# Kernel tuning notes

Hardware: AMD Instinct MI355X
Metric: run time of the kernel (lower is better)

## Reference

```python
import jax, jax.numpy as jnp
import numpy as np
from jax import lax

WHISPER_DIM, WAVLM_DIM, MUQ_DIM = 1280, 1024, 1024
CODEBOOK_SIZE, CODEBOOK_DIM = 8192, 256
B, T_W, T_M = 8, 2048, 1024  # T_w = T_wl = 2048 @50Hz, muq @25Hz -> T_m = 1024
CONCAT_DIM = WHISPER_DIM + WAVLM_DIM + MUQ_DIM


def setup_inputs() -> dict:
    key = jax.random.key(0)
    ks = jax.random.split(key, 10)
    s = 0.02
    return {
        "whisper_feat": jax.random.normal(ks[0], (B, T_W, WHISPER_DIM), jnp.float32),
        "wavlm_feat": jax.random.normal(ks[1], (B, T_W, WAVLM_DIM), jnp.float32),
        "muq_feat": jax.random.normal(ks[2], (B, T_M, MUQ_DIM), jnp.float32),
        # Conv1d weights, torch layout (out_ch, in_ch, k)
        "w_conv_w": jax.random.normal(ks[3], (WHISPER_DIM, WHISPER_DIM, 4), jnp.float32) * s,
        "w_conv_b": jnp.zeros((WHISPER_DIM,), jnp.float32),
        "wl_conv_w": jax.random.normal(ks[4], (WAVLM_DIM, WAVLM_DIM, 4), jnp.float32) * s,
        "wl_conv_b": jnp.zeros((WAVLM_DIM,), jnp.float32),
        # Linear: torch layout (out_features, in_features)
        "proj_w": jax.random.normal(ks[5], (CODEBOOK_DIM, CONCAT_DIM), jnp.float32) * s,
        "proj_b": jnp.zeros((CODEBOOK_DIM,), jnp.float32),
        "codebook": jax.random.normal(ks[6], (CODEBOOK_SIZE, CODEBOOK_DIM), jnp.float32) * 0.02,
    }


def _conv1d_s2(x_btc, w_oik, b):
    # x: (B, T, C) -> (B, C, T) conv k=4 s=2 p=1 -> (B, T//2, C)
    y = lax.conv_general_dilated(
        x_btc.transpose(0, 2, 1), w_oik,
        window_strides=(2,), padding=[(1, 1)],
        dimension_numbers=("NCH", "OIH", "NCH"))
    return (y + b[None, :, None]).transpose(0, 2, 1)


def reference(whisper_feat, wavlm_feat, muq_feat, w_conv_w, w_conv_b,
              wl_conv_w, wl_conv_b, proj_w, proj_b, codebook):
    w = _conv1d_s2(whisper_feat, w_conv_w, w_conv_b)   # (B, 1024, 1280)
    wl = _conv1d_s2(wavlm_feat, wl_conv_w, wl_conv_b)  # (B, 1024, 1024)
    m = muq_feat                                        # (B, 1024, 1024)
    min_len = min(w.shape[1], wl.shape[1], m.shape[1])
    concat = jnp.concatenate([w[:, :min_len], wl[:, :min_len], m[:, :min_len]], axis=-1)
    z_e = jnp.einsum("btc,dc->btd", concat, proj_w) + proj_b  # (B, T, D)

    # VQ: squared-Euclidean argmin against the codebook (same argmin as cdist)
    Bsz, T, D = z_e.shape
    z_flat = z_e.reshape(-1, D)
    d2 = (jnp.sum(z_flat * z_flat, axis=-1, keepdims=True)
          - 2.0 * z_flat @ codebook.T
          + jnp.sum(codebook * codebook, axis=-1)[None, :])  # (B*T, K)
    codes = jnp.argmin(d2, axis=-1)                     # (B*T,)
    z_q = codebook[codes].reshape(Bsz, T, D)
    z_q_st = z_e + lax.stop_gradient(z_q - z_e)
    commit_loss = jnp.mean(jnp.square(z_e - lax.stop_gradient(z_q)))
    return z_q_st, codes.reshape(Bsz, T), commit_loss
```

## Files before the change

### kernel.cpp

```cpp
#include <hip/hip_runtime.h>
#include <cstdint>
#include <cstddef>

typedef unsigned short u16;
typedef __attribute__((ext_vector_type(8))) short bf16x8;
typedef __attribute__((ext_vector_type(4))) float f32x4;
typedef unsigned int u32;
typedef __attribute__((address_space(1))) const u32 gu32;
typedef __attribute__((address_space(3))) u32 lu32;

__device__ __forceinline__ void gload_lds16(const void* g, void* l) {
    __builtin_amdgcn_global_load_lds((gu32*)g, (lu32*)l, 16, 0, 0);
}

__device__ __forceinline__ u16 f2bf(float v) {
    u32 u = __float_as_uint(v);
    return (u16)((u + 0x7fffu + ((u >> 16) & 1u)) >> 16);
}
__device__ __forceinline__ float bf2f(u16 h) { return __uint_as_float(((u32)h) << 16); }

__device__ __forceinline__ void split3(float f, u16& h1, u16& h2, u16& h3) {
    h1 = f2bf(f); float r = f - bf2f(h1);
    h2 = f2bf(r); r -= bf2f(h2);
    h3 = f2bf(r);
}

__device__ __forceinline__ void mfma6(f32x4& c, bf16x8 a1, bf16x8 a2, bf16x8 a3,
                                      bf16x8 b1, bf16x8 b2, bf16x8 b3) {
    c = __builtin_amdgcn_mfma_f32_16x16x32_bf16(a1, b1, c, 0, 0, 0);
    c = __builtin_amdgcn_mfma_f32_16x16x32_bf16(a1, b2, c, 0, 0, 0);
    c = __builtin_amdgcn_mfma_f32_16x16x32_bf16(a2, b1, c, 0, 0, 0);
    c = __builtin_amdgcn_mfma_f32_16x16x32_bf16(a1, b3, c, 0, 0, 0);
    c = __builtin_amdgcn_mfma_f32_16x16x32_bf16(a3, b1, c, 0, 0, 0);
    c = __builtin_amdgcn_mfma_f32_16x16x32_bf16(a2, b2, c, 0, 0, 0);
}

__global__ __launch_bounds__(256)
void split_x8t(const float* __restrict__ x, u16* __restrict__ p0,
               size_t pstr, int I) {
    __shared__ u16 tl[12288];
    const int b = blockIdx.x / 33, blk = blockIdx.x - b * 33;
    const int o0 = blk * 64;
    const int nval = (o0 + 64 <= 2050) ? 64 : (2050 - o0);
    const int c0 = blockIdx.y << 6;
    const int tid = threadIdx.x;
    const int r = tid >> 2, c4 = tid & 3;

    if (r < nval) {
        int local = o0 + r;
        int parity = local >= 1025 ? 1 : 0;
        int idx = local - parity * 1025;
        int prow = 2 * idx + parity;
        bool pad = (prow == 0) || (prow == 2049);
        int s = pad ? 0 : (prow - 1);
        const float* src = x + (size_t)(b * 2048 + s) * I + c0;
#pragma unroll
        for (int k = 0; k < 4; k++) {
            int cf4 = c4 + k * 4;
            float4 v = make_float4(0.f, 0.f, 0.f, 0.f);
            if (!pad) v = *reinterpret_cast<const float4*>(src + cf4 * 4);
            float vals[4] = {v.x, v.y, v.z, v.w};
            int base = ((cf4 >> 1) * 64 + r) * 8 + (cf4 & 1) * 4;
#pragma unroll
            for (int q = 0; q < 4; q++) {
                u16 h1, h2, h3; split3(vals[q], h1, h2, h3);
                tl[base + q]        = h1;
                tl[4096 + base + q] = h2;
                tl[8192 + base + q] = h3;
            }
        }
    }
    __syncthreads();
#pragma unroll
    for (int e = tid; e < 1536; e += 256) {
        int p = e >> 9, rem = e & 511;
        int gs = rem >> 6, rr = rem & 63;
        if (rr < nval) {
            size_t dst = (size_t)p * pstr +
                         (size_t)((c0 >> 3) + gs) * 131200 +
                         (size_t)(b * 2050 + o0 + rr) * 8;
            *reinterpret_cast<bf16x8*>(&p0[dst]) =
                *reinterpret_cast<const bf16x8*>(&tl[p * 4096 + (gs * 64 + rr) * 8]);
        }
    }
}

__global__ __launch_bounds__(256)
void split_rows8t(const float* __restrict__ in, u16* __restrict__ p0,
                  size_t pstr, int R, int C) {
    __shared__ u16 tl[12288];
    const int r0 = blockIdx.x << 6;
    const int c0 = blockIdx.y << 6;
    const int tid = threadIdx.x;
    const int r = tid >> 2, c4 = tid & 3;
    const float* src = in + (size_t)(r0 + r) * C + c0;
#pragma unroll
    for (int k = 0; k < 4; k++) {
        int cf4 = c4 + k * 4;
        float4 v = *reinterpret_cast<const float4*>(src + cf4 * 4);
        float vals[4] = {v.x, v.y, v.z, v.w};
        int base = ((cf4 >> 1) * 64 + r) * 8 + (cf4 & 1) * 4;
#pragma unroll
        for (int q = 0; q < 4; q++) {
            u16 h1, h2, h3; split3(vals[q], h1, h2, h3);
            tl[base + q]        = h1;
            tl[4096 + base + q] = h2;
            tl[8192 + base + q] = h3;
        }
    }
    __syncthreads();
#pragma unroll
    for (int e = tid; e < 1536; e += 256) {
        int p = e >> 9, rem = e & 511;
        int gs = rem >> 6, rr = rem & 63;
        size_t dst = (size_t)p * pstr +
                     ((size_t)((c0 >> 3) + gs) * R + (r0 + rr)) * 8;
        *reinterpret_cast<bf16x8*>(&p0[dst]) =
            *reinterpret_cast<const bf16x8*>(&tl[p * 4096 + (gs * 64 + rr) * 8]);
    }
}

__global__ __launch_bounds__(256)
void split_weightT8m(const float* __restrict__ w, u16* __restrict__ p0,
                     size_t pstr, int I, int O, int NT) {
    __shared__ u16 tl[12288];
    const int o0 = blockIdx.x << 6;
    const int c0 = blockIdx.y << 6;
    const int G = I >> 3;
    const size_t SLAB = (size_t)4 * G * NT * 8;
    const int tid = threadIdx.x;
    const int r = tid >> 2, c4 = tid & 3;
    for (int kcv = 0; kcv < 4; kcv++) {
#pragma unroll
        for (int k = 0; k < 4; k++) {
            int cf4 = c4 + k * 4;
#pragma unroll
            for (int q = 0; q < 4; q++) {
                int i = c0 + cf4 * 4 + q;
                float f = w[((size_t)(o0 + r) * I + i) * 4 + kcv];
                u16 h1, h2, h3; split3(f, h1, h2, h3);
                int base = ((cf4 >> 1) * 64 + r) * 8 + (cf4 & 1) * 4 + q;
                tl[base]        = h1;
                tl[4096 + base] = h2;
                tl[8192 + base] = h3;
            }
        }
        __syncthreads();
        for (int e = tid; e < 1536; e += 256) {
            int p = e >> 9, rem = e & 511;
            int gs = rem >> 6, rr = rem & 63;
            int o = o0 + rr;
            int ng = o / NT, orr = o - ng * NT;
            int kg = kcv * G + (c0 >> 3) + gs;
            size_t dst = (size_t)p * pstr + (size_t)ng * SLAB +
                         (size_t)kg * NT * 8 + (size_t)orr * 8;
            *reinterpret_cast<bf16x8*>(&p0[dst]) =
                *reinterpret_cast<const bf16x8*>(&tl[p * 4096 + (gs * 64 + rr) * 8]);
        }
        __syncthreads();
    }
}

__global__ void cnorm_kernel(const float* __restrict__ cb, float* __restrict__ cn) {
    int w = threadIdx.x >> 6, lane = threadIdx.x & 63;
    int row = blockIdx.x * 4 + w;
    float4 v = *reinterpret_cast<const float4*>(&cb[(size_t)row * 256 + lane * 4]);
    float s = v.x * v.x + v.y * v.y + v.z * v.z + v.w * v.w;
#pragma unroll
    for (int off = 32; off; off >>= 1) s += __shfl_xor(s, off);
    if (lane == 0) cn[row] = s;
}

template<int TN>
__global__ __launch_bounds__(256, 2)
void conv_mfma7(const u16* __restrict__ xs, unsigned pstr_x,
                const u16* __restrict__ wt, unsigned pstr_w,
                const float* __restrict__ bias,
                u16* __restrict__ outp, unsigned pstr_o,
                int I, int O) {
    constexpr int FN = TN / 32;
    constexpr int NB = TN / 16;
    constexpr int BPLANE = 32 * TN;
    constexpr int BUFE = 8192 + 2 * BPLANE;
    __shared__ u16 lds[2 * BUFE];
    const int m0 = blockIdx.x << 7;
    const int ny = blockIdx.y;
    const int n0 = ny * TN;
    const int tid = threadIdx.x, lane = tid & 63, wv = tid >> 6;
    const int wr = ((wv >> 1) & 1) << 6, wc = (wv & 1) * (TN / 2);
    const int fr = lane & 15, fkg = lane >> 4;
    const int b = m0 >> 10, t0 = m0 & 1023;
    const int G = I >> 3;
    const int SL = 131200;
    const int NIT = G, npt = G >> 2;
    const size_t SLAB = (size_t)4 * G * TN * 8;

    const u16* srcp[NB];
    int dsto[NB];
    const int nload = (wv < 2) ? 8 : NB;
    int inc;
    if (wv < 2) {
        inc = 4 * SL;
#pragma unroll
        for (int j = 0; j < NB; j++) {
            if (j < 8) {
                int kg = j >> 1, half = j & 1;
                int r = half * 64 + lane;
                srcp[j] = xs + (size_t)wv * pstr_x + (size_t)kg * SL +
                          (size_t)(b * 2050 + t0 + r) * 8;
                dsto[j] = wv * 4096 + j * 512;
            } else { srcp[j] = xs; dsto[j] = 0; }
        }
    } else {
        inc = BPLANE;
#pragma unroll
        for (int j = 0; j < NB; j++) {
            srcp[j] = wt + (size_t)(wv - 2) * pstr_w + (size_t)ny * SLAB +
                      j * 512 + lane * 8;
            dsto[j] = 8192 + (wv - 2) * BPLANE + j * 512;
        }
    }

    const u16* pa3 = xs + 2 * (size_t)pstr_x + (size_t)fkg * SL +
                     (size_t)(b * 2050 + t0 + wr + fr) * 8;
    const u16* pb3 = wt + 2 * (size_t)pstr_w + (size_t)ny * SLAB +
                     (size_t)fkg * (TN * 8) + (size_t)(wc + fr) * 8;

    f32x4 acc[4][FN];
#pragma unroll
    for (int i = 0; i < 4; i++)
#pragma unroll
        for (int j = 0; j < FN; j++) acc[i][j] = (f32x4){0.f, 0.f, 0.f, 0.f};

#pragma unroll
    for (int j = 0; j < NB; j++)
        if (j < nload) { gload_lds16(srcp[j], &lds[dsto[j]]); srcp[j] += inc; }
    __syncthreads();

    int scnt = npt - 1, skcv = 0;
    int dcnt = npt, dkcv = 0;
    int cur = 0;

    for (int it = 0; it < NIT; ++it) {
        const u16* lb = &lds[cur * BUFE];
        bf16x8 a1[4], a2[4], b1[FN], b2[FN];
#pragma unroll
        for (int fm = 0; fm < 4; fm++) {
            int aidx = fkg * 1024 + (wr + fm * 16 + fr) * 8;
            a1[fm] = *reinterpret_cast<const bf16x8*>(lb + aidx);
            a2[fm] = *reinterpret_cast<const bf16x8*>(lb + 4096 + aidx);
        }
#pragma unroll
        for (int fn = 0; fn < FN; fn++) {
            int bidx = 8192 + fkg * (TN * 8) + (wc + fn * 16 + fr) * 8;
            b1[fn] = *reinterpret_cast<const bf16x8*>(lb + bidx);
            b2[fn] = *reinterpret_cast<const bf16x8*>(lb + BPLANE + bidx);
        }
        if (it + 1 < NIT) {
#pragma unroll
            for (int j = 0; j < NB; j++)
                if (j < nload) {
                    gload_lds16(srcp[j], &lds[(cur ^ 1) * BUFE + dsto[j]]);
                    srcp[j] += inc;
                }
            if (wv < 2) {
                if (--scnt == 0) {
                    int d = ((skcv == 1) ? -8192 : 8200) - (int)pstr_x;
#pragma unroll
                    for (int j = 0; j < 8; j++) srcp[j] += d;
                    skcv++; scnt = npt;
                }
            }
        }
        bf16x8 da3[4], db3[FN];
#pragma unroll
        for (int fm = 0; fm < 4; fm++)
            da3[fm] = *reinterpret_cast<const bf16x8*>(pa3 + fm * 128);
#pragma unroll
        for (int fn = 0; fn < FN; fn++)
            db3[fn] = *reinterpret_cast<const bf16x8*>(pb3 + fn * 128);
        pa3 += 4 * SL;
        pb3 += BPLANE;
        if (--dcnt == 0) {
            pa3 += ((dkcv == 1) ? -8192 : 8200) - (int)pstr_x;
            dkcv++; dcnt = npt;
        }
        __builtin_amdgcn_s_setprio(1);
#pragma unroll
        for (int fm = 0; fm < 4; fm++)
#pragma unroll
            for (int fn = 0; fn < FN; fn++)
                mfma6(acc[fm][fn], a1[fm], a2[fm], da3[fm],
                      b1[fn], b2[fn], db3[fn]);
        __builtin_amdgcn_s_setprio(0);
        __syncthreads();
        cur ^= 1;
    }

    u16 (*eld)[32][TN + 8] = (u16 (*)[32][TN + 8])lds;
    float bv[FN];
#pragma unroll
    for (int fn = 0; fn < FN; fn++) bv[fn] = bias[n0 + wc + fn * 16 + fr];
    const int srb = (wr >> 6) * 16 + fkg * 4;
#pragma unroll
    for (int fm = 0; fm < 4; fm++) {
#pragma unroll
        for (int fn = 0; fn < FN; fn++) {
            int cl = wc + fn * 16 + fr;
#pragma unroll
            for (int j = 0; j < 4; j++) {
                float f = acc[fm][fn][j] + bv[fn];
                u16 h1, h2, h3; split3(f, h1, h2, h3);
                eld[0][srb + j][cl] = h1;
                eld[1][srb + j][cl] = h2;
                eld[2][srb + j][cl] = h3;
            }
        }
        __syncthreads();
        for (int e = tid; e < 96 * (TN / 8); e += 256) {
            int g = e / 96, rem = e - g * 96;
            int p = rem >> 5, sr = rem & 31;
            bf16x8 vv = *reinterpret_cast<const bf16x8*>(&eld[p][sr][g * 8]);
            int rowg = m0 + ((sr >> 4) << 6) + fm * 16 + (sr & 15);
            size_t addr = (size_t)p * pstr_o +
                          (size_t)((n0 >> 3) + g) * 65536 + (size_t)rowg * 8;
            *reinterpret_cast<bf16x8*>(&outp[addr]) = vv;
        }
        __syncthreads();
    }
}

__global__ __launch_bounds__(256, 3)
void proj_mfma5(const u16* __restrict__ sA, const u16* __restrict__ sB,
                const u16* __restrict__ sM, const u16* __restrict__ wp,
                const float* __restrict__ bias, float* __restrict__ z_e,
                u16* __restrict__ zpl) {
    __shared__ u16 lds[24576];
    const int m0 = blockIdx.x << 7;
    const int n0 = blockIdx.y << 7;
    const int tid = threadIdx.x, lane = tid & 63, wv = tid >> 6;
    const int wr = ((wv >> 1) & 1) << 6, wc = (wv & 1) << 6;
    const int fr = lane & 15, fkg = lane >> 4;

    const u16* srcp[12];
    int dsto[12];
#pragma unroll
    for (int j = 0; j < 12; j++) {
        int ii = wv * 12 + j;
        int tile = ii >> 3, sub = ii & 7;
        int kg = sub >> 1, half = sub & 1;
        int r = half * 64 + lane;
        if (tile >= 3)
            srcp[j] = wp + (size_t)(tile - 3) * 851968 + (size_t)kg * 2048 +
                      (size_t)(n0 + r) * 8;
        else
            srcp[j] = nullptr;
        dsto[j] = tile * 4096 + sub * 512;
    }

    f32x4 acc[4][4];
#pragma unroll
    for (int i = 0; i < 4; i++)
#pragma unroll
        for (int j = 0; j < 4; j++) acc[i][j] = (f32x4){0.f, 0.f, 0.f, 0.f};

    const u16* segp[3] = {sA, sB, sM};
    const int segG[3] = {160, 128, 128};
    const unsigned segP[3] = {10485760u, 8388608u, 8388608u};

    for (int seg = 0; seg < 3; seg++) {
        const u16* sp = segp[seg];
        const unsigned sps = segP[seg];
#pragma unroll
        for (int j = 0; j < 12; j++) {
            int ii = wv * 12 + j;
            int tile = ii >> 3, sub = ii & 7;
            int kg = sub >> 1, half = sub & 1;
            int r = half * 64 + lane;
            if (tile < 3)
                srcp[j] = sp + (size_t)tile * sps + (size_t)kg * 65536 +
                          (size_t)(m0 + r) * 8;
        }
        const int niter = segG[seg] >> 2;
        for (int it = 0; it < niter; it++) {
#pragma unroll
            for (int j = 0; j < 12; j++) {
                gload_lds16(srcp[j], &lds[dsto[j]]);
                int ii = wv * 12 + j;
                srcp[j] += (ii >> 3) < 3 ? 262144 : 8192;
            }
            __syncthreads();
            bf16x8 bfr[3][4];
#pragma unroll
            for (int p = 0; p < 3; p++)
#pragma unroll
                for (int fn = 0; fn < 4; fn++)
                    bfr[p][fn] = *reinterpret_cast<const bf16x8*>(
                        &lds[(3 + p) * 4096 + fkg * 1024 + (wc + fn * 16 + fr) * 8]);
            __builtin_amdgcn_s_setprio(1);
#pragma unroll
            for (int fm = 0; fm < 4; fm++) {
                int aidx = fkg * 1024 + (wr + fm * 16 + fr) * 8;
                bf16x8 a1 = *reinterpret_cast<const bf16x8*>(&lds[aidx]);
                bf16x8 a2 = *reinterpret_cast<const bf16x8*>(&lds[4096 + aidx]);
                bf16x8 a3 = *reinterpret_cast<const bf16x8*>(&lds[8192 + aidx]);
#pragma unroll
                for (int fn = 0; fn < 4; fn++)
                    mfma6(acc[fm][fn], a1, a2, a3, bfr[0][fn], bfr[1][fn], bfr[2][fn]);
            }
            __builtin_amdgcn_s_setprio(0);
            __syncthreads();
        }
    }
    u16 (*eld)[32][132] = (u16 (*)[32][132])lds;
    float bv[4];
#pragma unroll
    for (int fn = 0; fn < 4; fn++) bv[fn] = bias[n0 + wc + fn * 16 + fr];
    const int srb = (wr >> 6) * 16 + fkg * 4;
#pragma unroll
    for (int fm = 0; fm < 4; fm++) {
#pragma unroll
        for (int fn = 0; fn < 4; fn++) {
            int cl = wc + fn * 16 + fr;
            int col = n0 + cl;
#pragma unroll
            for (int j = 0; j < 4; j++) {
                float f = acc[fm][fn][j] + bv[fn];
                int rowg = m0 + wr + fm * 16 + fkg * 4 + j;
                z_e[(size_t)rowg * 256 + col] = f;
                u16 h1, h2, h3; split3(f, h1, h2, h3);
                eld[0][srb + j][cl] = h1;
                eld[1][srb + j][cl] = h2;
                eld[2][srb + j][cl] = h3;
            }
        }
        __syncthreads();
#pragma unroll
        for (int q = 0; q < 6; q++) {
            int e = q * 256 + tid;
            int g = e / 96, rem = e - g * 96;
            int p = rem >> 5, sr = rem & 31;
            bf16x8 vv = *reinterpret_cast<const bf16x8*>(&eld[p][sr][g * 8]);
            int rowg = m0 + ((sr >> 4) << 6) + fm * 16 + (sr & 15);
            size_t addr = (size_t)p * 2097152 +
                          (size_t)((n0 >> 3) + g) * 65536 + (size_t)rowg * 8;
            *reinterpret_cast<bf16x8*>(&zpl[addr]) = vv;
        }
        __syncthreads();
    }
}

__global__ __launch_bounds__(256, 2)
void vq_mfma5(const u16* __restrict__ zpl, const u16* __restrict__ cbpl,
              const float* __restrict__ cn, double* __restrict__ pmin,
              int* __restrict__ pidx) {
    __shared__ __align__(16) char smem[65536];
    u16* lds = (u16*)smem;
    const int m0 = blockIdx.x << 7;
    const int n0 = blockIdx.y << 7;
    const int tid = threadIdx.x, lane = tid & 63, wv = tid >> 6;
    const int wr = ((wv >> 1) & 1) << 6, wc = (wv & 1) << 6;
    const int fr = lane & 15, fkg = lane >> 4;

    const u16* srcp[8];
    int dsto[8];
    {
        const u16* bse = (wv < 2) ? (zpl + (size_t)wv * 2097152)
                                  : (cbpl + (size_t)(wv - 2) * 2097152);
        int r0 = (wv < 2) ? m0 : n0;
#pragma unroll
        for (int j = 0; j < 8; j++) {
            int kg = j >> 1, half = j & 1;
            srcp[j] = bse + (size_t)kg * 65536 + (size_t)(r0 + half * 64 + lane) * 8;
            dsto[j] = wv * 4096 + j * 512;
        }
    }
    const u16* pa3 = zpl + (size_t)2 * 2097152 + (size_t)fkg * 65536 +
                     (size_t)(m0 + wr + fr) * 8;
    const u16* pb3 = cbpl + (size_t)2 * 2097152 + (size_t)fkg * 65536 +
                     (size_t)(n0 + wc + fr) * 8;

    f32x4 acc[4][4];
#pragma unroll
    for (int i = 0; i < 4; i++)
#pragma unroll
        for (int j = 0; j < 4; j++) acc[i][j] = (f32x4){0.f, 0.f, 0.f, 0.f};

#pragma unroll
    for (int j = 0; j < 8; j++) {
        gload_lds16(srcp[j], &lds[dsto[j]]);
        srcp[j] += 262144;
    }
    __syncthreads();

    int cur = 0;
    for (int it = 0; it < 8; ++it) {
        const u16* lb = &lds[cur * 16384];
        bf16x8 a1[4], a2[4], b1[4], b2[4];
#pragma unroll
        for (int fm = 0; fm < 4; fm++) {
            int aidx = fkg * 1024 + (wr + fm * 16 + fr) * 8;
            a1[fm] = *reinterpret_cast<const bf16x8*>(lb + aidx);
            a2[fm] = *reinterpret_cast<const bf16x8*>(lb + 4096 + aidx);
        }
#pragma unroll
        for (int fn = 0; fn < 4; fn++) {
            int bidx = fkg * 1024 + (wc + fn * 16 + fr) * 8;
            b1[fn] = *reinterpret_cast<const bf16x8*>(lb + 8192 + bidx);
            b2[fn] = *reinterpret_cast<const bf16x8*>(lb + 12288 + bidx);
        }
        if (it + 1 < 8) {
#pragma unroll
            for (int j = 0; j < 8; j++) {
                gload_lds16(srcp[j], &lds[(cur ^ 1) * 16384 + dsto[j]]);
                srcp[j] += 262144;
            }
        }
        bf16x8 da3[4], db3[4];
#pragma unroll
        for (int fm = 0; fm < 4; fm++)
            da3[fm] = *reinterpret_cast<const bf16x8*>(pa3 + fm * 128);
#pragma unroll
        for (int fn = 0; fn < 4; fn++)
            db3[fn] = *reinterpret_cast<const bf16x8*>(pb3 + fn * 128);
        pa3 += 262144;
        pb3 += 262144;
        __builtin_amdgcn_s_setprio(1);
#pragma unroll
        for (int fm = 0; fm < 4; fm++)
#pragma unroll
            for (int fn = 0; fn < 4; fn++)
                mfma6(acc[fm][fn], a1[fm], a2[fm], da3[fm],
                      b1[fn], b2[fn], db3[fn]);
        __builtin_amdgcn_s_setprio(0);
        __syncthreads();
        cur ^= 1;
    }

    double (*red_d)[32] = (double (*)[32])smem;
    int (*red_n)[32] = (int (*)[32])(smem + 32768);
#pragma unroll
    for (int fm = 0; fm < 4; fm++)
#pragma unroll
        for (int j = 0; j < 4; j++) {
            double best = 1e300; int bestn = 0x7fffffff;
#pragma unroll
            for (int fn = 0; fn < 4; fn++) {
                int gn = n0 + wc + fn * 16 + fr;
                double d = (double)cn[gn] - 2.0 * (double)acc[fm][fn][j];
                if (d < best || (d == best && gn < bestn)) { best = d; bestn = gn; }
            }
            int row = wr + fm * 16 + fkg * 4 + j;
            int cand = ((wv & 1) << 4) + fr;
            red_d[row][cand] = best; red_n[row][cand] = bestn;
        }
    __syncthreads();
    if (tid < 128) {
        double best = red_d[tid][0]; int bestn = red_n[tid][0];
#pragma unroll 4
        for (int k = 1; k < 32; k++) {
            double d = red_d[tid][k]; int n2 = red_n[tid][k];
            if (d < best || (d == best && n2 < bestn)) { best = d; bestn = n2; }
        }
        size_t idx = (size_t)(m0 + tid) * 64 + (n0 >> 7);
        pmin[idx] = best; pidx[idx] = bestn;
    }
}

__global__ void vq_finalize(const double* __restrict__ pmin, const int* __restrict__ pidx,
                            const float* __restrict__ z, const float* __restrict__ cb,
                            float* __restrict__ out, double* __restrict__ cpart) {
    int w = threadIdx.x >> 6, lane = threadIdx.x & 63;
    int m = blockIdx.x * 4 + w;
    double d = pmin[(size_t)m * 64 + lane];
    int n = pidx[(size_t)m * 64 + lane];
#pragma unroll
    for (int off = 32; off; off >>= 1) {
        double d2 = __shfl_xor(d, off);
        int n2 = __shfl_xor(n, off);
        if (d2 < d || (d2 == d && n2 < n)) { d = d2; n = n2; }
    }
    float4 cv = *reinterpret_cast<const float4*>(&cb[(size_t)n * 256 + lane * 4]);
    float4 zv = *reinterpret_cast<const float4*>(&z[(size_t)m * 256 + lane * 4]);
    *reinterpret_cast<float4*>(&out[(size_t)m * 256 + lane * 4]) = cv;
    float dx = zv.x - cv.x, dy = zv.y - cv.y, dz = zv.z - cv.z, dw = zv.w - cv.w;
    double s = (double)(dx * dx) + (double)(dy * dy) + (double)(dz * dz) + (double)(dw * dw);
#pragma unroll
    for (int off = 32; off; off >>= 1) s += __shfl_xor(s, off);
    if (lane == 0) {
        out[2097152 + m] = (float)n;
        cpart[m] = s;
    }
}

__global__ void vq_reduce(const double* __restrict__ cpart, float* __restrict__ out) {
    __shared__ double sm[256];
    double s = 0.0;
    for (int i = threadIdx.x; i < 8192; i += 256) s += cpart[i];
    sm[threadIdx.x] = s;
    __syncthreads();
    for (int off = 128; off; off >>= 1) {
        if ((int)threadIdx.x < off) sm[threadIdx.x] += sm[threadIdx.x + off];
        __syncthreads();
    }
    if (threadIdx.x == 0) out[2105344] = (float)(sm[0] / 2097152.0);
}

extern "C" void kernel_launch(void* const* d_in, const int* in_sizes, int n_in,
                              void* d_out, int out_size, void* d_ws, size_t ws_size,
                              hipStream_t stream) {
    (void)in_sizes; (void)n_in; (void)out_size; (void)ws_size;
    const float* whisper   = (const float*)d_in[0];
    const float* wavlm     = (const float*)d_in[1];
    const float* muq       = (const float*)d_in[2];
    const float* w_conv_w  = (const float*)d_in[3];
    const float* w_conv_b  = (const float*)d_in[4];
    const float* wl_conv_w = (const float*)d_in[5];
    const float* wl_conv_b = (const float*)d_in[6];
    const float* proj_w    = (const float*)d_in[7];
    const float* proj_b    = (const float*)d_in[8];
    const float* codebook  = (const float*)d_in[9];
    float* out = (float*)d_out;
    char* wsb = (char*)d_ws;

    u16*   xsA   = (u16*)(wsb + 0);
    u16*   wtbA  = (u16*)(wsb + 125952000);
    u16*   cApl  = (u16*)(wsb + 176259072);
    u16*   xsB   = (u16*)(wsb + 0);
    u16*   wtbB  = (u16*)(wsb + 100761600);
    u16*   cBpl  = (u16*)(wsb + 125927424);
    u16*   muqpl = (u16*)(wsb + 0);
    u16*   wtpPl = (u16*)(wsb + 50331648);
    float* z_e   = (float*)(wsb + 55443456);
    u16*   zpl   = (u16*)(wsb + 63832064);
    u16*   cbpl  = (u16*)(wsb + 76414976);
    float* cnorm = (float*)(wsb + 88997888);
    double* pmin = (double*)(wsb + 89030656);
    int*    pidx = (int*)(wsb + 93224960);
    double* cpart= (double*)(wsb + 95322112);

    split_x8t<<<dim3(264, 20), 256, 0, stream>>>(whisper, xsA, 20992000, 1280);
    split_weightT8m<<<dim3(20, 20), 256, 0, stream>>>(w_conv_w, wtbA, 6553600,
                                                      1280, 1280, 160);
    conv_mfma7<160><<<dim3(64, 8), 256, 0, stream>>>(xsA, 20992000, wtbA, 6553600,
                                                     w_conv_b, cApl, 10485760,
                                                     1280, 1280);
    split_x8t<<<dim3(264, 16), 256, 0, stream>>>(wavlm, xsB, 16793600, 1024);
    split_weightT8m<<<dim3(16, 16), 256, 0, stream>>>(wl_conv_w, wtbB, 4194304,
                                                      1024, 1024, 128);
    conv_mfma7<128><<<dim3(64, 8), 256, 0, stream>>>(xsB, 16793600, wtbB, 4194304,
                                                     wl_conv_b, cBpl, 8388608,
                                                     1024, 1024);
    split_rows8t<<<dim3(128, 16), 256, 0, stream>>>(muq, muqpl, 8388608, 8192, 1024);
    split_rows8t<<<dim3(4, 52), 256, 0, stream>>>(proj_w, wtpPl, 851968, 256, 3328);
    proj_mfma5<<<dim3(64, 2), 256, 0, stream>>>(cApl, cBpl, muqpl, wtpPl, proj_b, z_e, zpl);
    split_rows8t<<<dim3(128, 4), 256, 0, stream>>>(codebook, cbpl, 2097152, 8192, 256);
    cnorm_kernel<<<2048, 256, 0, stream>>>(codebook, cnorm);
    vq_mfma5<<<dim3(64, 64), 256, 0, stream>>>(zpl, cbpl, cnorm, pmin, pidx);
    vq_finalize<<<2048, 256, 0, stream>>>(pmin, pidx, z_e, codebook, out, cpart);
    vq_reduce<<<1, 256, 0, stream>>>(cpart, out);
}
```

Measured before the change: 1.243 ms.

## Prefetch third-plane global fragments one iteration ahead in conv and VQ kernels

Result: slower. 1.362 ms (+9.6%).

```diff
diff --git a/kernel.cpp b/kernel.cpp
--- a/kernel.cpp
+++ b/kernel.cpp
@@ -173,7 +173,7 @@
 
 template<int TN>
 __global__ __launch_bounds__(256, 2)
-void conv_mfma7(const u16* __restrict__ xs, unsigned pstr_x,
+void conv_mfma8(const u16* __restrict__ xs, unsigned pstr_x,
                 const u16* __restrict__ wt, unsigned pstr_w,
                 const float* __restrict__ bias,
                 u16* __restrict__ outp, unsigned pstr_o,
@@ -232,69 +232,83 @@
 #pragma unroll
         for (int j = 0; j < FN; j++) acc[i][j] = (f32x4){0.f, 0.f, 0.f, 0.f};
 
+    int scnt = npt - 1, skcv = 0;
+    int dcnt = npt, dkcv = 0;
+
 #pragma unroll
     for (int j = 0; j < NB; j++)
         if (j < nload) { gload_lds16(srcp[j], &lds[dsto[j]]); srcp[j] += inc; }
+    bf16x8 daA[4], dbA[FN], daB[4], dbB[FN];
+#pragma unroll
+    for (int fm = 0; fm < 4; fm++)
+        daA[fm] = *reinterpret_cast<const bf16x8*>(pa3 + fm * 128);
+#pragma unroll
+    for (int fn = 0; fn < FN; fn++)
+        dbA[fn] = *reinterpret_cast<const bf16x8*>(pb3 + fn * 128);
+    pa3 += 4 * SL;
+    pb3 += BPLANE;
+    if (--dcnt == 0) {
+        pa3 += ((dkcv == 1) ? -8192 : 8200) - (int)pstr_x;
+        dkcv++; dcnt = npt;
+    }
     __syncthreads();
 
-    int scnt = npt - 1, skcv = 0;
-    int dcnt = npt, dkcv = 0;
-    int cur = 0;
-
-    for (int it = 0; it < NIT; ++it) {
-        const u16* lb = &lds[cur * BUFE];
-        bf16x8 a1[4], a2[4], b1[FN], b2[FN];
-#pragma unroll
-        for (int fm = 0; fm < 4; fm++) {
-            int aidx = fkg * 1024 + (wr + fm * 16 + fr) * 8;
-            a1[fm] = *reinterpret_cast<const bf16x8*>(lb + aidx);
-            a2[fm] = *reinterpret_cast<const bf16x8*>(lb + 4096 + aidx);
-        }
-#pragma unroll
-        for (int fn = 0; fn < FN; fn++) {
-            int bidx = 8192 + fkg * (TN * 8) + (wc + fn * 16 + fr) * 8;
-            b1[fn] = *reinterpret_cast<const bf16x8*>(lb + bidx);
-            b2[fn] = *reinterpret_cast<const bf16x8*>(lb + BPLANE + bidx);
-        }
-        if (it + 1 < NIT) {
-#pragma unroll
-            for (int j = 0; j < NB; j++)
-                if (j < nload) {
-                    gload_lds16(srcp[j], &lds[(cur ^ 1) * BUFE + dsto[j]]);
-                    srcp[j] += inc;
-                }
-            if (wv < 2) {
-                if (--scnt == 0) {
-                    int d = ((skcv == 1) ? -8192 : 8200) - (int)pstr_x;
-#pragma unroll
-                    for (int j = 0; j < 8; j++) srcp[j] += d;
-                    skcv++; scnt = npt;
-                }
-            }
-        }
-        bf16x8 da3[4], db3[FN];
+    auto subiter = [&](const u16* lbr, u16* lbw,
+                       bf16x8 (&daU)[4], bf16x8 (&dbU)[FN],
+                       bf16x8 (&daP)[4], bf16x8 (&dbP)[FN]) {
 #pragma unroll
         for (int fm = 0; fm < 4; fm++)
-            da3[fm] = *reinterpret_cast<const bf16x8*>(pa3 + fm * 128);
+            daP[fm] = *reinterpret_cast<const bf16x8*>(pa3 + fm * 128);
 #pragma unroll
         for (int fn = 0; fn < FN; fn++)
-            db3[fn] = *reinterpret_cast<const bf16x8*>(pb3 + fn * 128);
+            dbP[fn] = *reinterpret_cast<const bf16x8*>(pb3 + fn * 128);
         pa3 += 4 * SL;
         pb3 += BPLANE;
         if (--dcnt == 0) {
             pa3 += ((dkcv == 1) ? -8192 : 8200) - (int)pstr_x;
             dkcv++; dcnt = npt;
         }
+#pragma unroll
+        for (int j = 0; j < NB; j++)
+            if (j < nload) {
+                gload_lds16(srcp[j], lbw + dsto[j]);
+                srcp[j] += inc;
+            }
+        if (wv < 2) {
+            if (--scnt == 0) {
+                int d = ((skcv == 1) ? -8192 : 8200) - (int)pstr_x;
+#pragma unroll
+                for (int j = 0; j < 8; j++) srcp[j] += d;
+                skcv++; scnt = npt;
+            }
+        }
+        bf16x8 a1[4], a2[4], b1[FN], b2[FN];
+#pragma unroll
+        for (int fm = 0; fm < 4; fm++) {
+            int aidx = fkg * 1024 + (wr + fm * 16 + fr) * 8;
+            a1[fm] = *reinterpret_cast<const bf16x8*>(lbr + aidx);
+            a2[fm] = *reinterpret_cast<const bf16x8*>(lbr + 4096 + aidx);
+        }
+#pragma unroll
+        for (int fn = 0; fn < FN; fn++) {
+            int bidx = 8192 + fkg * (TN * 8) + (wc + fn * 16 + fr) * 8;
+            b1[fn] = *reinterpret_cast<const bf16x8*>(lbr + bidx);
+            b2[fn] = *reinterpret_cast<const bf16x8*>(lbr + BPLANE + bidx);
+        }
         __builtin_amdgcn_s_setprio(1);
 #pragma unroll
         for (int fm = 0; fm < 4; fm++)
 #pragma unroll
             for (int fn = 0; fn < FN; fn++)
-                mfma6(acc[fm][fn], a1[fm], a2[fm], da3[fm],
-                      b1[fn], b2[fn], db3[fn]);
+                mfma6(acc[fm][fn], a1[fm], a2[fm], daU[fm],
+                      b1[fn], b2[fn], dbU[fn]);
         __builtin_amdgcn_s_setprio(0);
         __syncthreads();
-        cur ^= 1;
+    };
+
+    for (int it = 0; it < NIT; it += 2) {
+        subiter(lds, lds + BUFE, daA, dbA, daB, dbB);
+        subiter(lds + BUFE, lds, daB, dbB, daA, dbA);
     }
 
     u16 (*eld)[32][TN + 8] = (u16 (*)[32][TN + 8])lds;
@@ -451,7 +465,7 @@
 }
 
 __global__ __launch_bounds__(256, 2)
-void vq_mfma5(const u16* __restrict__ zpl, const u16* __restrict__ cbpl,
+void vq_mfma6(const u16* __restrict__ zpl, const u16* __restrict__ cbpl,
               const float* __restrict__ cn, double* __restrict__ pmin,
               int* __restrict__ pidx) {
     __shared__ __align__(16) char smem[65536];
@@ -491,50 +505,60 @@
         gload_lds16(srcp[j], &lds[dsto[j]]);
         srcp[j] += 262144;
     }
+    bf16x8 daA[4], dbA[4], daB[4], dbB[4];
+#pragma unroll
+    for (int fm = 0; fm < 4; fm++)
+        daA[fm] = *reinterpret_cast<const bf16x8*>(pa3 + fm * 128);
+#pragma unroll
+    for (int fn = 0; fn < 4; fn++)
+        dbA[fn] = *reinterpret_cast<const bf16x8*>(pb3 + fn * 128);
+    pa3 += 262144;
+    pb3 += 262144;
     __syncthreads();
 
-    int cur = 0;
-    for (int it = 0; it < 8; ++it) {
-        const u16* lb = &lds[cur * 16384];
+    auto subiter = [&](const u16* lbr, u16* lbw,
+                       bf16x8 (&daU)[4], bf16x8 (&dbU)[4],
+                       bf16x8 (&daP)[4], bf16x8 (&dbP)[4]) {
+#pragma unroll
+        for (int fm = 0; fm < 4; fm++)
+            daP[fm] = *reinterpret_cast<const bf16x8*>(pa3 + fm * 128);
+#pragma unroll
+        for (int fn = 0; fn < 4; fn++)
+            dbP[fn] = *reinterpret_cast<const bf16x8*>(pb3 + fn * 128);
+        pa3 += 262144;
+        pb3 += 262144;
+#pragma unroll
+        for (int j = 0; j < 8; j++) {
+            gload_lds16(srcp[j], lbw + dsto[j]);
+            srcp[j] += 262144;
+        }
         bf16x8 a1[4], a2[4], b1[4], b2[4];
 #pragma unroll
         for (int fm = 0; fm < 4; fm++) {
             int aidx = fkg * 1024 + (wr + fm * 16 + fr) * 8;
-            a1[fm] = *reinterpret_cast<const bf16x8*>(lb + aidx);
-            a2[fm] = *reinterpret_cast<const bf16x8*>(lb + 4096 + aidx);
+            a1[fm] = *reinterpret_cast<const bf16x8*>(lbr + aidx);
+            a2[fm] = *reinterpret_cast<const bf16x8*>(lbr + 4096 + aidx);
         }
 #pragma unroll
         for (int fn = 0; fn < 4; fn++) {
             int bidx = fkg * 1024 + (wc + fn * 16 + fr) * 8;
-            b1[fn] = *reinterpret_cast<const bf16x8*>(lb + 8192 + bidx);
-            b2[fn] = *reinterpret_cast<const bf16x8*>(lb + 12288 + bidx);
-        }
-        if (it + 1 < 8) {
-#pragma unroll
-            for (int j = 0; j < 8; j++) {
-                gload_lds16(srcp[j], &lds[(cur ^ 1) * 16384 + dsto[j]]);
-                srcp[j] += 262144;
-            }
-        }
-        bf16x8 da3[4], db3[4];
+            b1[fn] = *reinterpret_cast<const bf16x8*>(lbr + 8192 + bidx);
+            b2[fn] = *reinterpret_cast<const bf16x8*>(lbr + 12288 + bidx);
+        }
+        __builtin_amdgcn_s_setprio(1);
 #pragma unroll
         for (int fm = 0; fm < 4; fm++)
-            da3[fm] = *reinterpret_cast<const bf16x8*>(pa3 + fm * 128);
-#pragma unroll
-        for (int fn = 0; fn < 4; fn++)
-            db3[fn] = *reinterpret_cast<const bf16x8*>(pb3 + fn * 128);
-        pa3 += 262144;
-        pb3 += 262144;
-        __builtin_amdgcn_s_setprio(1);
-#pragma unroll
-        for (int fm = 0; fm < 4; fm++)
 #pragma unroll
             for (int fn = 0; fn < 4; fn++)
-                mfma6(acc[fm][fn], a1[fm], a2[fm], da3[fm],
-                      b1[fn], b2[fn], db3[fn]);
+                mfma6(acc[fm][fn], a1[fm], a2[fm], daU[fm],
+                      b1[fn], b2[fn], dbU[fn]);
         __builtin_amdgcn_s_setprio(0);
         __syncthreads();
-        cur ^= 1;
+    };
+
+    for (int it = 0; it < 8; it += 2) {
+        subiter(lds, lds + 16384, daA, dbA, daB, dbB);
+        subiter(lds + 16384, lds, daB, dbB, daA, dbA);
     }
 
     double (*red_d)[32] = (double (*)[32])smem;
@@ -642,13 +666,13 @@
     split_x8t<<<dim3(264, 20), 256, 0, stream>>>(whisper, xsA, 20992000, 1280);
     split_weightT8m<<<dim3(20, 20), 256, 0, stream>>>(w_conv_w, wtbA, 6553600,
                                                       1280, 1280, 160);
-    conv_mfma7<160><<<dim3(64, 8), 256, 0, stream>>>(xsA, 20992000, wtbA, 6553600,
+    conv_mfma8<160><<<dim3(64, 8), 256, 0, stream>>>(xsA, 20992000, wtbA, 6553600,
                                                      w_conv_b, cApl, 10485760,
                                                      1280, 1280);
     split_x8t<<<dim3(264, 16), 256, 0, stream>>>(wavlm, xsB, 16793600, 1024);
     split_weightT8m<<<dim3(16, 16), 256, 0, stream>>>(wl_conv_w, wtbB, 4194304,
                                                       1024, 1024, 128);
-    conv_mfma7<128><<<dim3(64, 8), 256, 0, stream>>>(xsB, 16793600, wtbB, 4194304,
+    conv_mfma8<128><<<dim3(64, 8), 256, 0, stream>>>(xsB, 16793600, wtbB, 4194304,
                                                      wl_conv_b, cBpl, 8388608,
                                                      1024, 1024);
     split_rows8t<<<dim3(128, 16), 256, 0, stream>>>(muq, muqpl, 8388608, 8192, 1024);
@@ -656,7 +680,7 @@
     proj_mfma5<<<dim3(64, 2), 256, 0, stream>>>(cApl, cBpl, muqpl, wtpPl, proj_b, z_e, zpl);
     split_rows8t<<<dim3(128, 4), 256, 0, stream>>>(codebook, cbpl, 2097152, 8192, 256);
     cnorm_kernel<<<2048, 256, 0, stream>>>(codebook, cnorm);
-    vq_mfma5<<<dim3(64, 64), 256, 0, stream>>>(zpl, cbpl, cnorm, pmin, pidx);
+    vq_mfma6<<<dim3(64, 64), 256, 0, stream>>>(zpl, cbpl, cnorm, pmin, pidx);
     vq_finalize<<<2048, 256, 0, stream>>>(pmin, pidx, z_e, codebook, out, cpart);
     vq_reduce<<<1, 256, 0, stream>>>(cpart, out);
 }
```
